# Kernel optimization log

Hardware: AMD Instinct MI355X
Metric: run time of the kernel (lower is better)

## Reference

```python
import jax, jax.numpy as jnp
import numpy as np

EPS = 1e-09  # from module __init__ eps


def setup_inputs() -> dict:
    key = jax.random.key(0)
    k1, k2 = jax.random.split(key)
    N = 384 * 384
    input1 = jax.random.normal(k1, (1, 32, 384, 384), dtype=jnp.float32)
    input2 = jax.random.randint(k2, (N, 48), 0, N, dtype=jnp.int64)
    return {"input1": input1, "input2": input2}


def reference(input1, input2):
    # input1: [*, a, b, c] -> UU: [N, a] with N = b*c (pixels), a = features
    a, b, c = input1.shape[1], input1.shape[2], input1.shape[3]
    UU = input1.reshape(a, b * c).T  # [N, a]
    J = input2.shape[0]
    nbr = UU[input2]                      # [J, K, a] gather of neighbor features
    diff = UU[:J][:, None, :] - nbr       # [J, K, a]
    msd = jnp.mean(diff * diff, axis=-1)  # [J, K] mean squared distance
    D = -jnp.sqrt(msd + EPS)              # [J, K]
    W = jax.nn.softmax(D, axis=1)         # softmax over K neighbors
    return W
```

## Files before the change

### kernel.cpp

```cpp
#include <hip/hip_runtime.h>
#include <hip/hip_fp16.h>


#define EPS 1e-9f

typedef _Float16 h2 __attribute__((ext_vector_type(2)));
union V16 { uint4 u; h2 h[4]; };

__global__ __launch_bounds__(256) void transpose_half_kernel(
    const float* __restrict__ in, _Float16* __restrict__ UU, int N) {
  const int p = blockIdx.x * 256 + threadIdx.x;
  if (p >= N) return;
  __half h[32];
#pragma unroll
  for (int f = 0; f < 32; ++f) h[f] = __float2half_rn(in[(size_t)f * N + p]);
  uint4* dst = (uint4*)(UU + (size_t)p * 32);
#pragma unroll
  for (int r = 0; r < 4; ++r) {
    __half2 a = __halves2half2(h[8 * r + 0], h[8 * r + 1]);
    __half2 b = __halves2half2(h[8 * r + 2], h[8 * r + 3]);
    __half2 c = __halves2half2(h[8 * r + 4], h[8 * r + 5]);
    __half2 d = __halves2half2(h[8 * r + 6], h[8 * r + 7]);
    dst[r] = make_uint4(*(unsigned*)&a, *(unsigned*)&b, *(unsigned*)&c, *(unsigned*)&d);
  }
}

__device__ __forceinline__ float dot2acc(h2 d, float s) {
#if __has_builtin(__builtin_amdgcn_fdot2)
  return __builtin_amdgcn_fdot2(d, d, s, false);
#else
  float x = (float)d.x, y = (float)d.y;
  return s + x * x + y * y;
#endif
}

__global__ __launch_bounds__(256) void dist_softmax_kernel(
    const _Float16* __restrict__ UU, const int* __restrict__ idx,
    float* __restrict__ out, int J) {
  const int wave = blockIdx.x * 4 + (threadIdx.x >> 6);
  const int lane = threadIdx.x & 63;
  const int jA = wave * 2;
  const int jB = jA + 1;
  if (jA >= J) return;
  const int quad = lane >> 2;
  const int q = lane & 3;

  const int* iA = idx + (size_t)jA * 48;
  const int* iB = idx + (size_t)jB * 48;
  const int nA0 = iA[quad], nA1 = iA[16 + quad], nA2 = iA[32 + quad];
  const int nB0 = iB[quad], nB1 = iB[16 + quad], nB2 = iB[32 + quad];

  V16 aA, aB, bA0, bA1, bA2, bB0, bB1, bB2;
  aA.u = *(const uint4*)(UU + (size_t)jA * 32 + q * 8);
  aB.u = *(const uint4*)(UU + (size_t)jB * 32 + q * 8);
  bA0.u = *(const uint4*)(UU + (size_t)nA0 * 32 + q * 8);
  bA1.u = *(const uint4*)(UU + (size_t)nA1 * 32 + q * 8);
  bA2.u = *(const uint4*)(UU + (size_t)nA2 * 32 + q * 8);
  bB0.u = *(const uint4*)(UU + (size_t)nB0 * 32 + q * 8);
  bB1.u = *(const uint4*)(UU + (size_t)nB1 * 32 + q * 8);
  bB2.u = *(const uint4*)(UU + (size_t)nB2 * 32 + q * 8);

  float sA0 = 0.f, sA1 = 0.f, sA2 = 0.f;
  float sB0 = 0.f, sB1 = 0.f, sB2 = 0.f;
#pragma unroll
  for (int i = 0; i < 4; ++i) {
    const h2 avA = aA.h[i];
    const h2 avB = aB.h[i];
    sA0 = dot2acc(avA - bA0.h[i], sA0);
    sA1 = dot2acc(avA - bA1.h[i], sA1);
    sA2 = dot2acc(avA - bA2.h[i], sA2);
    sB0 = dot2acc(avB - bB0.h[i], sB0);
    sB1 = dot2acc(avB - bB1.h[i], sB1);
    sB2 = dot2acc(avB - bB2.h[i], sB2);
  }
  sA0 += __shfl_xor(sA0, 1); sA0 += __shfl_xor(sA0, 2);
  sA1 += __shfl_xor(sA1, 1); sA1 += __shfl_xor(sA1, 2);
  sA2 += __shfl_xor(sA2, 1); sA2 += __shfl_xor(sA2, 2);
  sB0 += __shfl_xor(sB0, 1); sB0 += __shfl_xor(sB0, 2);
  sB1 += __shfl_xor(sB1, 1); sB1 += __shfl_xor(sB1, 2);
  sB2 += __shfl_xor(sB2, 1); sB2 += __shfl_xor(sB2, 2);

  const float eA0 = __expf(-sqrtf(sA0 * (1.0f / 32.0f) + EPS));
  const float eA1 = __expf(-sqrtf(sA1 * (1.0f / 32.0f) + EPS));
  const float eA2 = __expf(-sqrtf(sA2 * (1.0f / 32.0f) + EPS));
  const float eB0 = __expf(-sqrtf(sB0 * (1.0f / 32.0f) + EPS));
  const float eB1 = __expf(-sqrtf(sB1 * (1.0f / 32.0f) + EPS));
  const float eB2 = __expf(-sqrtf(sB2 * (1.0f / 32.0f) + EPS));

  float tA = eA0 + eA1 + eA2;
  float tB = eB0 + eB1 + eB2;
#pragma unroll
  for (int off = 4; off < 64; off <<= 1) {
    tA += __shfl_xor(tA, off);
    tB += __shfl_xor(tB, off);
  }
  const float invA = 1.0f / tA;
  const float invB = 1.0f / tB;

  if (q == 0) {
    float* oA = out + (size_t)jA * 48;
    float* oB = out + (size_t)jB * 48;
    oA[quad] = eA0 * invA;
    oA[16 + quad] = eA1 * invA;
    oA[32 + quad] = eA2 * invA;
    oB[quad] = eB0 * invB;
    oB[16 + quad] = eB1 * invB;
    oB[32 + quad] = eB2 * invB;
  }
}

extern "C" void kernel_launch(void* const* d_in, const int* in_sizes, int n_in,
                              void* d_out, int out_size, void* d_ws, size_t ws_size,
                              hipStream_t stream) {
  const float* in1 = (const float*)d_in[0];
  const int* idx = (const int*)d_in[1];
  float* out = (float*)d_out;
  _Float16* UU = (_Float16*)d_ws;

  const int N = in_sizes[0] / 32;
  const int J = in_sizes[1] / 48;

  transpose_half_kernel<<<(N + 255) / 256, 256, 0, stream>>>(in1, UU, N);

  dist_softmax_kernel<<<(J + 7) / 8, 256, 0, stream>>>(UU, idx, out, J);
}
```

Measured before the change: 164.8 us.

## Make dist-softmax persistent with software-pipelined index and gather prefetch

Turns the distance/softmax kernel into a persistent grid-stride loop over row pairs with a fixed grid of 1024 blocks. The loop prefetches the next pair's gathers and the pair after that's indices while the current pair is computed, to hide gather latency. Index loads and output stores become nontemporal to avoid polluting cache. The added double-buffered registers may lower occupancy, a fixed grid can underfill the GPU, and an odd J would drop the last row.

```diff
diff --git a/kernel.cpp b/kernel.cpp
--- a/kernel.cpp
+++ b/kernel.cpp
@@ -34,44 +34,50 @@
 #endif
 }
 
-__global__ __launch_bounds__(256) void dist_softmax_kernel(
-    const _Float16* __restrict__ UU, const int* __restrict__ idx,
-    float* __restrict__ out, int J) {
-  const int wave = blockIdx.x * 4 + (threadIdx.x >> 6);
-  const int lane = threadIdx.x & 63;
-  const int jA = wave * 2;
-  const int jB = jA + 1;
-  if (jA >= J) return;
-  const int quad = lane >> 2;
-  const int q = lane & 3;
+struct Gather {
+  V16 aA, aB, bA0, bA1, bA2, bB0, bB1, bB2;
+};
 
-  const int* iA = idx + (size_t)jA * 48;
-  const int* iB = idx + (size_t)jB * 48;
-  const int nA0 = iA[quad], nA1 = iA[16 + quad], nA2 = iA[32 + quad];
-  const int nB0 = iB[quad], nB1 = iB[16 + quad], nB2 = iB[32 + quad];
+__device__ __forceinline__ void load_idx6(const int* __restrict__ idx, int pair,
+                                          int quad, int n[6]) {
+  const int* ij = idx + (size_t)(2 * pair) * 48;
+  n[0] = __builtin_nontemporal_load(ij + quad);
+  n[1] = __builtin_nontemporal_load(ij + 16 + quad);
+  n[2] = __builtin_nontemporal_load(ij + 32 + quad);
+  n[3] = __builtin_nontemporal_load(ij + 48 + quad);
+  n[4] = __builtin_nontemporal_load(ij + 64 + quad);
+  n[5] = __builtin_nontemporal_load(ij + 80 + quad);
+}
 
-  V16 aA, aB, bA0, bA1, bA2, bB0, bB1, bB2;
-  aA.u = *(const uint4*)(UU + (size_t)jA * 32 + q * 8);
-  aB.u = *(const uint4*)(UU + (size_t)jB * 32 + q * 8);
-  bA0.u = *(const uint4*)(UU + (size_t)nA0 * 32 + q * 8);
-  bA1.u = *(const uint4*)(UU + (size_t)nA1 * 32 + q * 8);
-  bA2.u = *(const uint4*)(UU + (size_t)nA2 * 32 + q * 8);
-  bB0.u = *(const uint4*)(UU + (size_t)nB0 * 32 + q * 8);
-  bB1.u = *(const uint4*)(UU + (size_t)nB1 * 32 + q * 8);
-  bB2.u = *(const uint4*)(UU + (size_t)nB2 * 32 + q * 8);
+__device__ __forceinline__ void issue_gathers(const _Float16* __restrict__ UU,
+                                              int pair, const int n[6], int q,
+                                              Gather& g) {
+  const int jA = 2 * pair;
+  g.aA.u = *(const uint4*)(UU + (size_t)jA * 32 + q * 8);
+  g.aB.u = *(const uint4*)(UU + (size_t)(jA + 1) * 32 + q * 8);
+  g.bA0.u = *(const uint4*)(UU + (size_t)n[0] * 32 + q * 8);
+  g.bA1.u = *(const uint4*)(UU + (size_t)n[1] * 32 + q * 8);
+  g.bA2.u = *(const uint4*)(UU + (size_t)n[2] * 32 + q * 8);
+  g.bB0.u = *(const uint4*)(UU + (size_t)n[3] * 32 + q * 8);
+  g.bB1.u = *(const uint4*)(UU + (size_t)n[4] * 32 + q * 8);
+  g.bB2.u = *(const uint4*)(UU + (size_t)n[5] * 32 + q * 8);
+}
 
+__device__ __forceinline__ void compute_store(const Gather& g,
+                                              float* __restrict__ out, int pair,
+                                              int quad, int q) {
   float sA0 = 0.f, sA1 = 0.f, sA2 = 0.f;
   float sB0 = 0.f, sB1 = 0.f, sB2 = 0.f;
 #pragma unroll
   for (int i = 0; i < 4; ++i) {
-    const h2 avA = aA.h[i];
-    const h2 avB = aB.h[i];
-    sA0 = dot2acc(avA - bA0.h[i], sA0);
-    sA1 = dot2acc(avA - bA1.h[i], sA1);
-    sA2 = dot2acc(avA - bA2.h[i], sA2);
-    sB0 = dot2acc(avB - bB0.h[i], sB0);
-    sB1 = dot2acc(avB - bB1.h[i], sB1);
-    sB2 = dot2acc(avB - bB2.h[i], sB2);
+    const h2 avA = g.aA.h[i];
+    const h2 avB = g.aB.h[i];
+    sA0 = dot2acc(avA - g.bA0.h[i], sA0);
+    sA1 = dot2acc(avA - g.bA1.h[i], sA1);
+    sA2 = dot2acc(avA - g.bA2.h[i], sA2);
+    sB0 = dot2acc(avB - g.bB0.h[i], sB0);
+    sB1 = dot2acc(avB - g.bB1.h[i], sB1);
+    sB2 = dot2acc(avB - g.bB2.h[i], sB2);
   }
   sA0 += __shfl_xor(sA0, 1); sA0 += __shfl_xor(sA0, 2);
   sA1 += __shfl_xor(sA1, 1); sA1 += __shfl_xor(sA1, 2);
@@ -98,14 +104,46 @@
   const float invB = 1.0f / tB;
 
   if (q == 0) {
-    float* oA = out + (size_t)jA * 48;
-    float* oB = out + (size_t)jB * 48;
-    oA[quad] = eA0 * invA;
-    oA[16 + quad] = eA1 * invA;
-    oA[32 + quad] = eA2 * invA;
-    oB[quad] = eB0 * invB;
-    oB[16 + quad] = eB1 * invB;
-    oB[32 + quad] = eB2 * invB;
+    float* oA = out + (size_t)(2 * pair) * 48;
+    __builtin_nontemporal_store(eA0 * invA, oA + quad);
+    __builtin_nontemporal_store(eA1 * invA, oA + 16 + quad);
+    __builtin_nontemporal_store(eA2 * invA, oA + 32 + quad);
+    float* oB = oA + 48;
+    __builtin_nontemporal_store(eB0 * invB, oB + quad);
+    __builtin_nontemporal_store(eB1 * invB, oB + 16 + quad);
+    __builtin_nontemporal_store(eB2 * invB, oB + 32 + quad);
+  }
+}
+
+__global__ __launch_bounds__(256, 4) void dist_softmax_kernel(
+    const _Float16* __restrict__ UU, const int* __restrict__ idx,
+    float* __restrict__ out, int P) {
+  const int W = gridDim.x * 4;
+  int p = blockIdx.x * 4 + (threadIdx.x >> 6);
+  const int lane = threadIdx.x & 63;
+  const int quad = lane >> 2;
+  const int q = lane & 3;
+  if (p >= P) return;
+
+  int icur[6], inxt[6];
+  Gather gcur, gnxt;
+
+  load_idx6(idx, p, quad, icur);
+  const int p1 = p + W;
+  if (p1 < P) load_idx6(idx, p1, quad, inxt);
+  issue_gathers(UU, p, icur, q, gcur);
+
+  while (true) {
+    const int pn = p + W;
+    if (pn < P) {
+      issue_gathers(UU, pn, inxt, q, gnxt);
+      const int pn2 = pn + W;
+      if (pn2 < P) load_idx6(idx, pn2, quad, inxt);
+    }
+    compute_store(gcur, out, p, quad, q);
+    if (pn >= P) break;
+    gcur = gnxt;
+    p = pn;
   }
 }
 
@@ -119,8 +157,11 @@
 
   const int N = in_sizes[0] / 32;
   const int J = in_sizes[1] / 48;
+  const int P = J / 2;
 
   transpose_half_kernel<<<(N + 255) / 256, 256, 0, stream>>>(in1, UU, N);
 
-  dist_softmax_kernel<<<(J + 7) / 8, 256, 0, stream>>>(UU, idx, out, J);
+  int blocks = 1024;
+  if (P < 4096) blocks = (P + 3) / 4;
+  dist_softmax_kernel<<<blocks, 256, 0, stream>>>(UU, idx, out, P);
 }
```

Measured after the change: 168.4 us. 1.02x slower.
